# Optimization experiments

Measured on AMD Instinct MI355X. Metric: run time of the kernel, lower is better.

## Reference

```python
import jax, jax.numpy as jnp
import numpy as np

N = 20000      # nodes
E = 320000     # edges
C = 8          # n_species (input 0e multiplicity)
H = 128        # hidden multiplicity per irrep
RB = 8         # radial basis size
RM = 64        # radial mlp width
CUTOFF = 5.0
P = 2.0        # polynomial cutoff power
AVG_N = 16.0   # avg_n_neighbors
SQRT3 = float(np.sqrt(3.0))


def _w(k, i, o, scale=1.0):
    return jax.random.normal(k, (i, o), jnp.float32) * np.sqrt(scale / i)


def setup_inputs() -> dict:
    key = jax.random.key(0)
    ks = jax.random.split(key, 24)
    return {
        'displacements': jax.random.normal(ks[0], (E, 3), jnp.float32) * 1.5,
        'species': jax.random.randint(ks[1], (N,), 0, C, dtype=jnp.int32),
        'senders': jax.random.randint(ks[2], (E,), 0, N, dtype=jnp.int32),
        'receivers': jax.random.randint(ks[3], (E,), 0, N, dtype=jnp.int32),
        'l1_lin1': _w(ks[4], C, C),
        'l1_rw0': _w(ks[5], RB, RM, 4.0),
        'l1_rw1': _w(ks[6], RM, RM, 4.0),
        'l1_rw2': _w(ks[7], RM, RM, 4.0),
        'l1_rw3': _w(ks[8], RM, 2 * C),
        'l1_w2s': _w(ks[9], C, 2 * H),
        'l1_w2v': _w(ks[10], C, H),
        'l1_skip': jax.random.normal(ks[11], (C, C, 2 * H), jnp.float32) / np.sqrt(C),
        'l2_lin1s': _w(ks[12], H, H),
        'l2_lin1v': _w(ks[13], H, H),
        'l2_rw0': _w(ks[14], RB, RM, 4.0),
        'l2_rw1': _w(ks[15], RM, RM, 4.0),
        'l2_rw2': _w(ks[16], RM, RM, 4.0),
        'l2_rw3': _w(ks[17], RM, 2 * H),
        'l2_w2': _w(ks[18], 2 * H, H),
        'l2_skip': jax.random.normal(ks[19], (C, H, H), jnp.float32) / np.sqrt(H),
        'readout_w': _w(ks[20], H, 1),
    }


def _bessel(x):
    w = jnp.linspace(1.0, RB, RB) * jnp.pi
    xs = x[:, None]
    safe = jnp.where(xs == 0.0, 1.0, xs)
    return (2.0 / CUTOFF) * jnp.where(xs == 0.0, w / CUTOFF, jnp.sin(w * xs / CUTOFF) / safe)


def _poly_cutoff(x):
    u = x / CUTOFF
    out = 1.0 - (P + 1.0) * (P + 2.0) / 2.0 * u ** P \
        + P * (P + 2.0) * u ** (P + 1.0) \
        - P * (P + 1.0) / 2.0 * u ** (P + 2.0)
    return out * jnp.where(u < 1.0, 1.0, 0.0)


def _radial(rb, w0, w1, w2, w3):
    h = jax.nn.silu(rb @ w0)
    h = jax.nn.silu(h @ w1)
    h = jax.nn.silu(h @ w2)
    return h @ w3


def _node_energies(displacements, species, senders, receivers,
                   l1_lin1, l1_rw0, l1_rw1, l1_rw2, l1_rw3, l1_w2s, l1_w2v, l1_skip,
                   l2_lin1s, l2_lin1v, l2_rw0, l2_rw1, l2_rw2, l2_rw3, l2_w2, l2_skip,
                   readout_w):
    sq = jnp.sum(displacements ** 2, axis=-1)
    rn = jnp.where(sq == 0.0, 0.0, jnp.sqrt(jnp.where(sq == 0.0, 1.0, sq)))
    rb = _bessel(rn) * _poly_cutoff(rn)[:, None]                     # (E,RB)
    unit = displacements / jnp.where(rn == 0.0, 1.0, rn)[:, None]
    Y1 = SQRT3 * unit                                                # 1o SH, component norm
    onehot = jax.nn.one_hot(species, C, dtype=displacements.dtype)   # (N,C) = Cx0e features
    inv_sqrt_nbr = 1.0 / np.sqrt(AVG_N)

    # ---- layer 1: Cx0e -> 128x0e + 128x1o ----
    s = (onehot @ l1_lin1)[senders]                                  # (E,C)
    R = _radial(rb, l1_rw0, l1_rw1, l1_rw2, l1_rw3)                  # (E,2C)
    msg_s = s * R[:, :C]                                             # 0e x 0e -> 0e
    msg_v = s[:, :, None] * Y1[:, None, :] * R[:, C:, None]          # 0e x 1o -> 1o (E,C,3)
    agg_s = jax.ops.segment_sum(msg_s, receivers, num_segments=N) * inv_sqrt_nbr
    agg_v = jax.ops.segment_sum(msg_v, receivers, num_segments=N) * inv_sqrt_nbr
    scal = agg_s @ l1_w2s + jnp.einsum('nc,ncd->nd', onehot, l1_skip[species])  # (N,2H)
    vec = jnp.einsum('nci,cd->ndi', agg_v, l1_w2v)                   # (N,H,3)
    # gate: first H even scalars -> silu, last H scalars gate the 1o vectors
    x0 = jax.nn.silu(scal[:, :H])
    x1 = vec * jax.nn.silu(scal[:, H:])[:, :, None]

    # ---- layer 2: 128x0e + 128x1o -> 128x0e ----
    s2 = (x0 @ l2_lin1s)[senders]                                    # (E,H)
    v2 = jnp.einsum('nci,cd->ndi', x1, l2_lin1v)[senders]            # (E,H,3)
    tp = jnp.concatenate([s2, jnp.einsum('eci,ei->ec', v2, Y1) / SQRT3], axis=-1)  # (E,2H)
    R2 = _radial(rb, l2_rw0, l2_rw1, l2_rw2, l2_rw3)                 # (E,2H)
    agg2 = jax.ops.segment_sum(tp * R2, receivers, num_segments=N) * inv_sqrt_nbr
    feat = jax.nn.silu(agg2 @ l2_w2 + jnp.einsum('nc,ncd->nd', x0, l2_skip[species]))

    return feat @ readout_w                                          # (N,1) node energies


def reference(displacements, l1_lin1, l1_rw0, l1_rw1, l1_rw2, l1_rw3, l1_w2s, l1_w2v,
              l1_skip, l2_lin1s, l2_lin1v, l2_rw0, l2_rw1, l2_rw2, l2_rw3, l2_w2,
              l2_skip, readout_w, species, senders, receivers):
    return _node_energies(displacements, species, senders, receivers,
                          l1_lin1, l1_rw0, l1_rw1, l1_rw2, l1_rw3, l1_w2s, l1_w2v, l1_skip,
                          l2_lin1s, l2_lin1v, l2_rw0, l2_rw1, l2_rw2, l2_rw3, l2_w2, l2_skip,
                          readout_w)
```

## Files before the change

kernel.cpp:

```cpp
#include <hip/hip_runtime.h>
#include <math.h>

#define NN_ 20000
#define EE_ 320000
#define SHP 68

__device__ __forceinline__ float silu_f(float x) { return x / (1.0f + expf(-x)); }

template<int KD>
__device__ __forceinline__ void layer_step(float* __restrict__ sh_h,
                                           const float* __restrict__ sh_w,
                                           int wavebase, int eg, int jg) {
  const int jb = jg * 8;
  float acc[8][8];
#pragma unroll
  for (int ee = 0; ee < 8; ++ee)
#pragma unroll
    for (int jj = 0; jj < 8; ++jj) acc[ee][jj] = 0.f;

#pragma unroll
  for (int kc = 0; kc < KD; kc += 4) {
    float4 w4[4][2];
#pragma unroll
    for (int kk = 0; kk < 4; ++kk) {
      w4[kk][0] = *(const float4*)&sh_w[(kc + kk) * 64 + jb];
      w4[kk][1] = *(const float4*)&sh_w[(kc + kk) * 64 + jb + 4];
    }
    float4 h4[8];
#pragma unroll
    for (int ee = 0; ee < 8; ++ee)
      h4[ee] = *(const float4*)&sh_h[(wavebase + eg + 8 * ee) * SHP + kc];
#pragma unroll
    for (int kk = 0; kk < 4; ++kk) {
#pragma unroll
      for (int ee = 0; ee < 8; ++ee) {
        const float hv = ((const float*)&h4[ee])[kk];
        acc[ee][0] = fmaf(hv, w4[kk][0].x, acc[ee][0]);
        acc[ee][1] = fmaf(hv, w4[kk][0].y, acc[ee][1]);
        acc[ee][2] = fmaf(hv, w4[kk][0].z, acc[ee][2]);
        acc[ee][3] = fmaf(hv, w4[kk][0].w, acc[ee][3]);
        acc[ee][4] = fmaf(hv, w4[kk][1].x, acc[ee][4]);
        acc[ee][5] = fmaf(hv, w4[kk][1].y, acc[ee][5]);
        acc[ee][6] = fmaf(hv, w4[kk][1].z, acc[ee][6]);
        acc[ee][7] = fmaf(hv, w4[kk][1].w, acc[ee][7]);
      }
    }
  }
#pragma unroll
  for (int ee = 0; ee < 8; ++ee) {
    float* dst = &sh_h[(wavebase + eg + 8 * ee) * SHP + jb];
    float4 lo = {silu_f(acc[ee][0]), silu_f(acc[ee][1]), silu_f(acc[ee][2]), silu_f(acc[ee][3])};
    float4 hi = {silu_f(acc[ee][4]), silu_f(acc[ee][5]), silu_f(acc[ee][6]), silu_f(acc[ee][7])};
    *(float4*)dst = lo;
    *(float4*)(dst + 4) = hi;
  }
}

__device__ __forceinline__ void load_w(const float* __restrict__ W, int nfloat,
                                       float* __restrict__ dst, int t) {
  for (int i = t * 4; i < nfloat; i += 512) *(float4*)(dst + i) = *(const float4*)(W + i);
}

__global__ __launch_bounds__(256) void k_hist(const int* __restrict__ receivers,
                                              int* __restrict__ hist) {
  const int e = blockIdx.x * 256 + threadIdx.x;
  atomicAdd(&hist[receivers[e]], 1);
}

__global__ __launch_bounds__(1024) void k_scan(const int* __restrict__ hist,
                                               int* __restrict__ offs,
                                               int* __restrict__ cursor) {
  __shared__ int lds[1024];
  __shared__ int carry_s;
  const int t = threadIdx.x;
  if (t == 0) carry_s = 0;
  __syncthreads();
  for (int base = 0; base < NN_; base += 1024) {
    const int i = base + t;
    const int v = (i < NN_) ? hist[i] : 0;
    lds[t] = v;
    __syncthreads();
    for (int d = 1; d < 1024; d <<= 1) {
      const int tv = (t >= d) ? lds[t - d] : 0;
      __syncthreads();
      lds[t] += tv;
      __syncthreads();
    }
    const int inc = lds[t];
    const int c = carry_s;
    if (i < NN_) {
      const int off = c + inc - v;
      offs[i] = off;
      cursor[i] = off;
    }
    __syncthreads();
    if (t == 0) carry_s = c + lds[1023];
    __syncthreads();
  }
  if (t == 0) offs[NN_] = carry_s;
}

__global__ __launch_bounds__(256) void k_scatter(const int* __restrict__ receivers,
                                                 int* __restrict__ cursor,
                                                 int* __restrict__ edge_id) {
  const int e = blockIdx.x * 256 + threadIdx.x;
  const int r = receivers[e];
  const int pos = atomicAdd(&cursor[r], 1);
  edge_id[pos] = e;
}

__global__ __launch_bounds__(128) void k1a_radial(
    const float* __restrict__ disp, const int* __restrict__ species,
    const int* __restrict__ senders,
    const float* __restrict__ lin1,
    const float* __restrict__ rw0, const float* __restrict__ rw1,
    const float* __restrict__ rw2, const float* __restrict__ rw3,
    float* __restrict__ buf1, float* __restrict__ rbc_g, float* __restrict__ y1_g) {
  __shared__ float sh_h[128 * SHP];
  __shared__ float sh_w[64 * 64];
  const int t = threadIdx.x;
  const int e0 = blockIdx.x * 128;
  const int e = e0 + t;

  const float dx = disp[e * 3 + 0], dy = disp[e * 3 + 1], dz = disp[e * 3 + 2];
  const float sq = dx * dx + dy * dy + dz * dz;
  const float rn = sqrtf(sq);
  const float inv = (rn == 0.f) ? 1.f : (1.f / rn);
  const float u = rn * 0.2f;
  float fc;
  {
    const float u2 = u * u;
    fc = 1.f - 6.f * u2 + 8.f * u2 * u - 3.f * u2 * u2;
    fc = (u < 1.f) ? fc : 0.f;
  }
  float rb[8];
#pragma unroll
  for (int k = 0; k < 8; ++k) {
    const float wk = (float)(k + 1) * 3.14159265358979323846f;
    const float s = (rn == 0.f) ? (wk * 0.2f) : (sinf(wk * u) * inv);
    rb[k] = 0.4f * s * fc;
  }
  float4 r0 = {rb[0], rb[1], rb[2], rb[3]};
  float4 r1 = {rb[4], rb[5], rb[6], rb[7]};
  *(float4*)(rbc_g + e * 8) = r0;
  *(float4*)(rbc_g + e * 8 + 4) = r1;
  const float y1x = 1.7320508075688772f * dx * inv;
  const float y1y = 1.7320508075688772f * dy * inv;
  const float y1z = 1.7320508075688772f * dz * inv;
  float4 y4 = {y1x, y1y, y1z, 0.f};
  *(float4*)(y1_g + e * 4) = y4;
  *(float4*)&sh_h[t * SHP] = r0;
  *(float4*)&sh_h[t * SHP + 4] = r1;

  const int wavebase = (t >> 6) * 64;
  const int lane = t & 63;
  const int eg = lane >> 3, jg = lane & 7;

  load_w(rw0, 8 * 64, sh_w, t);
  __syncthreads();
  layer_step<8>(sh_h, sh_w, wavebase, eg, jg);
  __syncthreads();
  load_w(rw1, 64 * 64, sh_w, t);
  __syncthreads();
  layer_step<64>(sh_h, sh_w, wavebase, eg, jg);
  __syncthreads();
  load_w(rw2, 64 * 64, sh_w, t);
  __syncthreads();
  layer_step<64>(sh_h, sh_w, wavebase, eg, jg);
  __syncthreads();

  float R[16];
#pragma unroll
  for (int c = 0; c < 16; ++c) R[c] = 0.f;
  for (int k = 0; k < 64; ++k) {
    const float h = sh_h[t * SHP + k];
#pragma unroll
    for (int c = 0; c < 16; ++c) R[c] = fmaf(h, rw3[k * 16 + c], R[c]);
  }

  const int sp = species[senders[e]];
  float m[32];
#pragma unroll
  for (int c = 0; c < 8; ++c) {
    const float sc = lin1[sp * 8 + c];
    m[c] = sc * R[c];
    const float mv = sc * R[8 + c];
    m[8 + c * 3 + 0] = mv * y1x;
    m[8 + c * 3 + 1] = mv * y1y;
    m[8 + c * 3 + 2] = mv * y1z;
  }
  float* dst = buf1 + (size_t)e * 32;
#pragma unroll
  for (int q = 0; q < 8; ++q) {
    float4 v = {m[q * 4 + 0], m[q * 4 + 1], m[q * 4 + 2], m[q * 4 + 3]};
    *(float4*)(dst + q * 4) = v;
  }
}

__global__ __launch_bounds__(128) void k3a_radial(
    const float* __restrict__ rbc_g,
    const float* __restrict__ rw0, const float* __restrict__ rw1,
    const float* __restrict__ rw2,
    float* __restrict__ ha_buf) {
  __shared__ float sh_h[128 * SHP];
  __shared__ float sh_w[64 * 64];
  const int t = threadIdx.x;
  const int e0 = blockIdx.x * 128;

  *(float4*)&sh_h[t * SHP] = *(const float4*)(rbc_g + (size_t)(e0 + t) * 8);
  *(float4*)&sh_h[t * SHP + 4] = *(const float4*)(rbc_g + (size_t)(e0 + t) * 8 + 4);

  const int wavebase = (t >> 6) * 64;
  const int lane = t & 63;
  const int eg = lane >> 3, jg = lane & 7;

  load_w(rw0, 8 * 64, sh_w, t);
  __syncthreads();
  layer_step<8>(sh_h, sh_w, wavebase, eg, jg);
  __syncthreads();
  load_w(rw1, 64 * 64, sh_w, t);
  __syncthreads();
  layer_step<64>(sh_h, sh_w, wavebase, eg, jg);
  __syncthreads();
  load_w(rw2, 64 * 64, sh_w, t);
  __syncthreads();
  layer_step<64>(sh_h, sh_w, wavebase, eg, jg);
  __syncthreads();

#pragma unroll
  for (int r = 0; r < 16; ++r) {
    const int lin = r * 128 + t;
    const int el = lin >> 4;
    const int k = (lin & 15) * 4;
    *(float4*)(ha_buf + (size_t)(e0 + el) * 64 + k) = *(const float4*)&sh_h[el * SHP + k];
  }
}

__global__ __launch_bounds__(256) void k1b_gather(
    const float* __restrict__ buf1, const int* __restrict__ offs,
    const int* __restrict__ edge_id,
    float* __restrict__ agg_s, float* __restrict__ agg_v) {
  const int n = blockIdx.x * 8 + (threadIdx.x >> 5);
  const int ch = threadIdx.x & 31;
  const int beg = offs[n], end = offs[n + 1];
  float acc = 0.f;
  for (int i = beg; i < end; ++i) {
    const int eid = edge_id[i];
    acc += buf1[(size_t)eid * 32 + ch];
  }
  if (ch < 8) agg_s[n * 8 + ch] = acc;
  else agg_v[n * 24 + (ch - 8)] = acc;
}

__global__ __launch_bounds__(64) void k2a_node(
    const float* __restrict__ agg_s, const float* __restrict__ agg_v,
    const int* __restrict__ species,
    const float* __restrict__ w2s, const float* __restrict__ w2v,
    const float* __restrict__ skip1,
    float* __restrict__ x0_g, float* __restrict__ x1_g) {
  const int n = blockIdx.x;
  const int l = threadIdx.x;
  __shared__ float g_lds[128];
  const int sp = species[n];
  float as[8];
#pragma unroll
  for (int k = 0; k < 8; ++k) as[k] = agg_s[n * 8 + k] * 0.25f;
  float sc[4];
#pragma unroll
  for (int j = 0; j < 4; ++j) {
    const int d = l * 4 + j;
    float a = skip1[(sp * 9) * 256 + d];
#pragma unroll
    for (int k = 0; k < 8; ++k) a = fmaf(as[k], w2s[k * 256 + d], a);
    sc[j] = silu_f(a);
  }
  if (l < 32) {
#pragma unroll
    for (int j = 0; j < 4; ++j) x0_g[n * 128 + l * 4 + j] = sc[j];
  } else {
#pragma unroll
    for (int j = 0; j < 4; ++j) g_lds[(l - 32) * 4 + j] = sc[j];
  }
  __syncthreads();
  float av[24];
#pragma unroll
  for (int k = 0; k < 24; ++k) av[k] = agg_v[n * 24 + k] * 0.25f;
#pragma unroll
  for (int h = 0; h < 2; ++h) {
    const int d = l + h * 64;
    const float g = g_lds[d];
    float v0 = 0.f, v1 = 0.f, v2v = 0.f;
#pragma unroll
    for (int c = 0; c < 8; ++c) {
      const float w = w2v[c * 128 + d];
      v0 = fmaf(av[c * 3 + 0], w, v0);
      v1 = fmaf(av[c * 3 + 1], w, v1);
      v2v = fmaf(av[c * 3 + 2], w, v2v);
    }
    x1_g[(n * 3 + 0) * 128 + d] = v0 * g;
    x1_g[(n * 3 + 1) * 128 + d] = v1 * g;
    x1_g[(n * 3 + 2) * 128 + d] = v2v * g;
  }
}

__global__ __launch_bounds__(256) void k2b_gemm(
    const float* __restrict__ x0_g, const float* __restrict__ x1_g,
    const int* __restrict__ species,
    const float* __restrict__ lin1s, const float* __restrict__ lin1v,
    const float* __restrict__ skip2,
    float* __restrict__ s2_g, float* __restrict__ v2_g,
    float* __restrict__ skipv_g) {
  const int w = __builtin_amdgcn_readfirstlane((int)(threadIdx.x >> 6));
  const int l = threadIdx.x & 63;
  const int nbase = blockIdx.x * 32 + w * 8;
  float s2a[8] = {}, s2b[8] = {}, ska[8] = {}, skb[8] = {};
  float v2a[8][3] = {}, v2b[8][3] = {};
  int sp[8];
#pragma unroll
  for (int nn = 0; nn < 8; ++nn) sp[nn] = species[nbase + nn];
  for (int c = 0; c < 128; ++c) {
    const float wA0 = lin1s[c * 128 + l];
    const float wA1 = lin1s[c * 128 + 64 + l];
    const float wB0 = lin1v[c * 128 + l];
    const float wB1 = lin1v[c * 128 + 64 + l];
#pragma unroll
    for (int nn = 0; nn < 8; ++nn) {
      const int n = nbase + nn;
      const float x0v = x0_g[n * 128 + c];
      const float wS0 = skip2[sp[nn] * 16384 + c * 128 + l];
      const float wS1 = skip2[sp[nn] * 16384 + c * 128 + 64 + l];
      s2a[nn] = fmaf(x0v, wA0, s2a[nn]);
      s2b[nn] = fmaf(x0v, wA1, s2b[nn]);
      ska[nn] = fmaf(x0v, wS0, ska[nn]);
      skb[nn] = fmaf(x0v, wS1, skb[nn]);
#pragma unroll
      for (int i = 0; i < 3; ++i) {
        const float x1v = x1_g[(n * 3 + i) * 128 + c];
        v2a[nn][i] = fmaf(x1v, wB0, v2a[nn][i]);
        v2b[nn][i] = fmaf(x1v, wB1, v2b[nn][i]);
      }
    }
  }
#pragma unroll
  for (int nn = 0; nn < 8; ++nn) {
    const int n = nbase + nn;
    s2_g[n * 128 + l] = s2a[nn];
    s2_g[n * 128 + 64 + l] = s2b[nn];
    skipv_g[n * 128 + l] = ska[nn];
    skipv_g[n * 128 + 64 + l] = skb[nn];
#pragma unroll
    for (int i = 0; i < 3; ++i) {
      v2_g[n * 384 + l * 3 + i] = v2a[nn][i];
      v2_g[n * 384 + (64 + l) * 3 + i] = v2b[nn][i];
    }
  }
}

__global__ __launch_bounds__(256) void k3b_gather(
    const float* __restrict__ ha_buf, const float* __restrict__ y1_g,
    const int* __restrict__ senders,
    const int* __restrict__ offs, const int* __restrict__ edge_id,
    const float* __restrict__ rw3,
    const float* __restrict__ s2_g, const float* __restrict__ v2_g,
    float* __restrict__ agg2) {
  const int n = blockIdx.x;
  const int ch = threadIdx.x;
  float w[64];
#pragma unroll
  for (int k = 0; k < 64; ++k) w[k] = rw3[k * 256 + ch];
  const int beg = offs[n], end = offs[n + 1];
  const bool is_s = ch < 128;
  const int c3 = (ch - 128) * 3;
  float acc = 0.f;
  for (int i = beg; i < end; ++i) {
    const int eid = __builtin_amdgcn_readfirstlane(edge_id[i]);
    const int s = __builtin_amdgcn_readfirstlane(senders[eid]);
    const float y1x = y1_g[eid * 4 + 0];
    const float y1y = y1_g[eid * 4 + 1];
    const float y1z = y1_g[eid * 4 + 2];
    float tp;
    if (is_s) {
      tp = s2_g[(size_t)s * 128 + ch];
    } else {
      tp = (v2_g[(size_t)s * 384 + c3 + 0] * y1x +
            v2_g[(size_t)s * 384 + c3 + 1] * y1y +
            v2_g[(size_t)s * 384 + c3 + 2] * y1z) * 0.5773502691896258f;
    }
    const float* ha = ha_buf + (size_t)eid * 64;
    float r0 = 0.f, r1 = 0.f, r2 = 0.f, r3 = 0.f;
#pragma unroll
    for (int k = 0; k < 64; k += 4) {
      r0 = fmaf(ha[k + 0], w[k + 0], r0);
      r1 = fmaf(ha[k + 1], w[k + 1], r1);
      r2 = fmaf(ha[k + 2], w[k + 2], r2);
      r3 = fmaf(ha[k + 3], w[k + 3], r3);
    }
    acc = fmaf(tp, (r0 + r1) + (r2 + r3), acc);
  }
  agg2[(size_t)n * 256 + ch] = acc;
}

__global__ __launch_bounds__(256) void k4_node(
    const float* __restrict__ agg2, const float* __restrict__ skipv,
    const float* __restrict__ w2, const float* __restrict__ readout,
    float* __restrict__ out) {
  __shared__ float tile[64 * 65];
  __shared__ float partial[256];
  const int t = threadIdx.x;
  const int w = __builtin_amdgcn_readfirstlane((int)(threadIdx.x >> 6));
  const int l = t & 63;
  const int n0 = blockIdx.x * 64;
  const int n = n0 + l;
  float acc[32];
#pragma unroll
  for (int j = 0; j < 32; ++j) acc[j] = 0.f;
  for (int ko = 0; ko < 256; ko += 64) {
    __syncthreads();
#pragma unroll
    for (int rep = 0; rep < 16; ++rep) {
      const int lin = rep * 256 + t;
      const int node = lin >> 6, kk = lin & 63;
      const int gn = n0 + node;
      tile[kk * 65 + node] = (gn < NN_) ? agg2[(size_t)gn * 256 + ko + kk] * 0.25f : 0.f;
    }
    __syncthreads();
    for (int kk = 0; kk < 64; ++kk) {
      const float a = tile[kk * 65 + l];
#pragma unroll
      for (int jj = 0; jj < 32; ++jj)
        acc[jj] = fmaf(a, w2[(ko + kk) * 128 + w * 32 + jj], acc[jj]);
    }
  }
  float po = 0.f;
  if (n < NN_) {
#pragma unroll
    for (int jj = 0; jj < 32; ++jj) {
      const int d = w * 32 + jj;
      const float v = acc[jj] + skipv[n * 128 + d];
      po = fmaf(silu_f(v), readout[d], po);
    }
  }
  partial[w * 64 + l] = po;
  __syncthreads();
  if (t < 64 && n0 + t < NN_) {
    out[n0 + t] = partial[t] + partial[64 + t] + partial[128 + t] + partial[192 + t];
  }
}

extern "C" void kernel_launch(void* const* d_in, const int* in_sizes, int n_in,
                              void* d_out, int out_size, void* d_ws, size_t ws_size,
                              hipStream_t stream) {
  const float* disp = (const float*)d_in[0];
  const int* species = (const int*)d_in[1];
  const int* senders = (const int*)d_in[2];
  const int* receivers = (const int*)d_in[3];
  const float* l1_lin1 = (const float*)d_in[4];
  const float* l1_rw0 = (const float*)d_in[5];
  const float* l1_rw1 = (const float*)d_in[6];
  const float* l1_rw2 = (const float*)d_in[7];
  const float* l1_rw3 = (const float*)d_in[8];
  const float* l1_w2s = (const float*)d_in[9];
  const float* l1_w2v = (const float*)d_in[10];
  const float* l1_skip = (const float*)d_in[11];
  const float* l2_lin1s = (const float*)d_in[12];
  const float* l2_lin1v = (const float*)d_in[13];
  const float* l2_rw0 = (const float*)d_in[14];
  const float* l2_rw1 = (const float*)d_in[15];
  const float* l2_rw2 = (const float*)d_in[16];
  const float* l2_rw3 = (const float*)d_in[17];
  const float* l2_w2 = (const float*)d_in[18];
  const float* l2_skip = (const float*)d_in[19];
  const float* readout_w = (const float*)d_in[20];

  float* ws = (float*)d_ws;
  float* rbc   = ws;
  float* y1    = ws + 2560000;
  float* s2    = ws + 3840000;
  float* v2    = ws + 6400000;
  float* skipv = ws + 14080000;
  float* agg2  = ws + 16640000;
  float* pool  = ws + 21760000;
  float* agg_s = pool;
  float* agg_v = pool + 160000;
  float* buf1  = pool + 640000;
  float* x0    = pool + 640000;
  float* x1    = pool + 3200000;
  float* ha    = pool;
  int* ibase   = (int*)(ws + 42240000);
  int* hist    = ibase;
  int* cursor  = ibase + 20000;
  int* offs    = ibase + 40000;
  int* edge_id = ibase + 60001;
  if (ws_size < (size_t)(42240000 + 380001) * 4) return;

  hipMemsetAsync(hist, 0, 20000 * sizeof(int), stream);
  k_hist<<<EE_ / 256, 256, 0, stream>>>(receivers, hist);
  k_scan<<<1, 1024, 0, stream>>>(hist, offs, cursor);
  k_scatter<<<EE_ / 256, 256, 0, stream>>>(receivers, cursor, edge_id);

  k1a_radial<<<EE_ / 128, 128, 0, stream>>>(disp, species, senders, l1_lin1,
                                            l1_rw0, l1_rw1, l1_rw2, l1_rw3,
                                            buf1, rbc, y1);
  k1b_gather<<<NN_ / 8, 256, 0, stream>>>(buf1, offs, edge_id, agg_s, agg_v);
  k2a_node<<<NN_, 64, 0, stream>>>(agg_s, agg_v, species, l1_w2s, l1_w2v, l1_skip,
                                   x0, x1);
  k2b_gemm<<<NN_ / 32, 256, 0, stream>>>(x0, x1, species, l2_lin1s, l2_lin1v,
                                         l2_skip, s2, v2, skipv);

  k3a_radial<<<EE_ / 128, 128, 0, stream>>>(rbc, l2_rw0, l2_rw1, l2_rw2, ha);
  k3b_gather<<<NN_, 256, 0, stream>>>(ha, y1, senders, offs, edge_id, l2_rw3,
                                      s2, v2, agg2);
  k4_node<<<(NN_ + 63) / 64, 256, 0, stream>>>(agg2, skipv, l2_w2, readout_w,
                                               (float*)d_out);
}
```

Baseline: 1.092 ms.

## Stage per-edge radial hidden rows in LDS in batches of sixteen edges

The layer-2 gather kernel now loads the 64-wide hidden radial activations for up to 16 incoming edges cooperatively into shared memory with float4 loads. Each thread then reads them back as broadcast float4 LDS reads instead of every thread issuing scalar global loads per edge. The sender feature gathers for all 16 edges are issued before the compute loop so more memory requests are in flight at once. The cost is two block barriers per batch, extra registers for the tp array and the pinned float4 weights, and wasted lanes when a node has few neighbours.

```diff
diff --git a/kernel.cpp b/kernel.cpp
--- a/kernel.cpp
+++ b/kernel.cpp
@@ -6,6 +6,8 @@
 #define SHP 68
 
 __device__ __forceinline__ float silu_f(float x) { return x / (1.0f + expf(-x)); }
+
+#define KEEP4(v) asm volatile("" : "+v"(v.x), "+v"(v.y), "+v"(v.z), "+v"(v.w))
 
 template<int KD>
 __device__ __forceinline__ void layer_step(float* __restrict__ sh_h,
@@ -363,39 +365,71 @@
     const float* __restrict__ rw3,
     const float* __restrict__ s2_g, const float* __restrict__ v2_g,
     float* __restrict__ agg2) {
+  __shared__ float ha_lds[16][64];
   const int n = blockIdx.x;
   const int ch = threadIdx.x;
-  float w[64];
-#pragma unroll
-  for (int k = 0; k < 64; ++k) w[k] = rw3[k * 256 + ch];
+
+  float4 w4[16];
+#pragma unroll
+  for (int q = 0; q < 16; ++q) {
+    w4[q].x = rw3[(q * 4 + 0) * 256 + ch];
+    w4[q].y = rw3[(q * 4 + 1) * 256 + ch];
+    w4[q].z = rw3[(q * 4 + 2) * 256 + ch];
+    w4[q].w = rw3[(q * 4 + 3) * 256 + ch];
+    KEEP4(w4[q]);
+  }
+
   const int beg = offs[n], end = offs[n + 1];
   const bool is_s = ch < 128;
   const int c3 = (ch - 128) * 3;
+  const int be = ch >> 4;
+  const int k4 = (ch & 15) * 4;
   float acc = 0.f;
-  for (int i = beg; i < end; ++i) {
-    const int eid = __builtin_amdgcn_readfirstlane(edge_id[i]);
-    const int s = __builtin_amdgcn_readfirstlane(senders[eid]);
-    const float y1x = y1_g[eid * 4 + 0];
-    const float y1y = y1_g[eid * 4 + 1];
-    const float y1z = y1_g[eid * 4 + 2];
-    float tp;
-    if (is_s) {
-      tp = s2_g[(size_t)s * 128 + ch];
-    } else {
-      tp = (v2_g[(size_t)s * 384 + c3 + 0] * y1x +
-            v2_g[(size_t)s * 384 + c3 + 1] * y1y +
-            v2_g[(size_t)s * 384 + c3 + 2] * y1z) * 0.5773502691896258f;
-    }
-    const float* ha = ha_buf + (size_t)eid * 64;
-    float r0 = 0.f, r1 = 0.f, r2 = 0.f, r3 = 0.f;
-#pragma unroll
-    for (int k = 0; k < 64; k += 4) {
-      r0 = fmaf(ha[k + 0], w[k + 0], r0);
-      r1 = fmaf(ha[k + 1], w[k + 1], r1);
-      r2 = fmaf(ha[k + 2], w[k + 2], r2);
-      r3 = fmaf(ha[k + 3], w[k + 3], r3);
-    }
-    acc = fmaf(tp, (r0 + r1) + (r2 + r3), acc);
+
+  for (int b = beg; b < end; b += 16) {
+    const int nb = end - b;
+    __syncthreads();
+    float4 hv = {0.f, 0.f, 0.f, 0.f};
+    if (be < nb) {
+      const int eid = edge_id[b + be];
+      hv = *(const float4*)(ha_buf + (size_t)eid * 64 + k4);
+    }
+    *(float4*)&ha_lds[be][k4] = hv;
+    float tp[16];
+#pragma unroll
+    for (int j = 0; j < 16; ++j) {
+      tp[j] = 0.f;
+      if (j < nb) {
+        const int eid = __builtin_amdgcn_readfirstlane(edge_id[b + j]);
+        const int s = __builtin_amdgcn_readfirstlane(senders[eid]);
+        if (is_s) {
+          tp[j] = s2_g[(size_t)s * 128 + ch];
+        } else {
+          const float y1x = y1_g[eid * 4 + 0];
+          const float y1y = y1_g[eid * 4 + 1];
+          const float y1z = y1_g[eid * 4 + 2];
+          tp[j] = (v2_g[(size_t)s * 384 + c3 + 0] * y1x +
+                   v2_g[(size_t)s * 384 + c3 + 1] * y1y +
+                   v2_g[(size_t)s * 384 + c3 + 2] * y1z) * 0.5773502691896258f;
+        }
+      }
+    }
+    __syncthreads();
+#pragma unroll
+    for (int j = 0; j < 16; ++j) {
+      if (j < nb) {
+        float d0 = 0.f, d1 = 0.f, d2 = 0.f, d3 = 0.f;
+#pragma unroll
+        for (int q = 0; q < 16; ++q) {
+          const float4 h = *(const float4*)&ha_lds[j][q * 4];
+          d0 = fmaf(h.x, w4[q].x, d0);
+          d1 = fmaf(h.y, w4[q].y, d1);
+          d2 = fmaf(h.z, w4[q].z, d2);
+          d3 = fmaf(h.w, w4[q].w, d3);
+        }
+        acc = fmaf(tp[j], (d0 + d1) + (d2 + d3), acc);
+      }
+    }
   }
   agg2[(size_t)n * 256 + ch] = acc;
 }
```

Result: slower. 1.410 ms (+29.1%).

## Move final radial layer into tiled GEMM and process edges in sorted phases

Applied to the files above, without the earlier changes.

The last radial-MLP layer (64->256) no longer runs as a per-edge register dot product inside the gather kernel. It now runs as a shared-memory tiled GEMM in the radial kernel, which reads edges in receiver-sorted order and writes the full 256-wide R2 rows to a buffer. Because that buffer is large, edges are handled in four phases of 80000. Each phase launches the radial GEMM and then a gather that adds each node's partial sums into a zeroed agg2. The aim is to remove the redundant per-node, per-channel 64-FMA work and the 64-register weight array in the gather, at the cost of about 80MB of extra R2 traffic per phase, eight extra launches, a memset and read-modify-write accumulation into agg2.

```diff
diff --git a/kernel.cpp b/kernel.cpp
--- a/kernel.cpp
+++ b/kernel.cpp
@@ -4,6 +4,7 @@
 #define NN_ 20000
 #define EE_ 320000
 #define SHP 68
+#define EPH 80000
 
 __device__ __forceinline__ float silu_f(float x) { return x / (1.0f + expf(-x)); }
 
@@ -51,6 +52,55 @@
     float* dst = &sh_h[(wavebase + eg + 8 * ee) * SHP + jb];
     float4 lo = {silu_f(acc[ee][0]), silu_f(acc[ee][1]), silu_f(acc[ee][2]), silu_f(acc[ee][3])};
     float4 hi = {silu_f(acc[ee][4]), silu_f(acc[ee][5]), silu_f(acc[ee][6]), silu_f(acc[ee][7])};
+    *(float4*)dst = lo;
+    *(float4*)(dst + 4) = hi;
+  }
+}
+
+__device__ __forceinline__ void gemm_chunk_out(const float* __restrict__ sh_h,
+                                               const float* __restrict__ sh_w,
+                                               int wavebase, int eg, int jg,
+                                               float* __restrict__ dst_base) {
+  const int jb = jg * 8;
+  float acc[8][8];
+#pragma unroll
+  for (int ee = 0; ee < 8; ++ee)
+#pragma unroll
+    for (int jj = 0; jj < 8; ++jj) acc[ee][jj] = 0.f;
+
+#pragma unroll
+  for (int kc = 0; kc < 64; kc += 4) {
+    float4 w4[4][2];
+#pragma unroll
+    for (int kk = 0; kk < 4; ++kk) {
+      w4[kk][0] = *(const float4*)&sh_w[(kc + kk) * 64 + jb];
+      w4[kk][1] = *(const float4*)&sh_w[(kc + kk) * 64 + jb + 4];
+    }
+    float4 h4[8];
+#pragma unroll
+    for (int ee = 0; ee < 8; ++ee)
+      h4[ee] = *(const float4*)&sh_h[(wavebase + eg + 8 * ee) * SHP + kc];
+#pragma unroll
+    for (int kk = 0; kk < 4; ++kk) {
+#pragma unroll
+      for (int ee = 0; ee < 8; ++ee) {
+        const float hv = ((const float*)&h4[ee])[kk];
+        acc[ee][0] = fmaf(hv, w4[kk][0].x, acc[ee][0]);
+        acc[ee][1] = fmaf(hv, w4[kk][0].y, acc[ee][1]);
+        acc[ee][2] = fmaf(hv, w4[kk][0].z, acc[ee][2]);
+        acc[ee][3] = fmaf(hv, w4[kk][0].w, acc[ee][3]);
+        acc[ee][4] = fmaf(hv, w4[kk][1].x, acc[ee][4]);
+        acc[ee][5] = fmaf(hv, w4[kk][1].y, acc[ee][5]);
+        acc[ee][6] = fmaf(hv, w4[kk][1].z, acc[ee][6]);
+        acc[ee][7] = fmaf(hv, w4[kk][1].w, acc[ee][7]);
+      }
+    }
+  }
+#pragma unroll
+  for (int ee = 0; ee < 8; ++ee) {
+    float* dst = dst_base + (size_t)(wavebase + eg + 8 * ee) * 256 + jb;
+    float4 lo = {acc[ee][0], acc[ee][1], acc[ee][2], acc[ee][3]};
+    float4 hi = {acc[ee][4], acc[ee][5], acc[ee][6], acc[ee][7]};
     *(float4*)dst = lo;
     *(float4*)(dst + 4) = hi;
   }
@@ -197,18 +247,19 @@
   }
 }
 
-__global__ __launch_bounds__(128) void k3a_radial(
-    const float* __restrict__ rbc_g,
+__global__ __launch_bounds__(128) void k3a_fused(
+    const float* __restrict__ rbc_g, const int* __restrict__ edge_id,
     const float* __restrict__ rw0, const float* __restrict__ rw1,
-    const float* __restrict__ rw2,
-    float* __restrict__ ha_buf) {
+    const float* __restrict__ rw2, const float* __restrict__ rw3,
+    float* __restrict__ r2buf, int pbase) {
   __shared__ float sh_h[128 * SHP];
   __shared__ float sh_w[64 * 64];
   const int t = threadIdx.x;
-  const int e0 = blockIdx.x * 128;
-
-  *(float4*)&sh_h[t * SHP] = *(const float4*)(rbc_g + (size_t)(e0 + t) * 8);
-  *(float4*)&sh_h[t * SHP + 4] = *(const float4*)(rbc_g + (size_t)(e0 + t) * 8 + 4);
+  const int p = pbase + blockIdx.x * 128 + t;
+  const int eid = edge_id[p];
+
+  *(float4*)&sh_h[t * SHP] = *(const float4*)(rbc_g + (size_t)eid * 8);
+  *(float4*)&sh_h[t * SHP + 4] = *(const float4*)(rbc_g + (size_t)eid * 8 + 4);
 
   const int wavebase = (t >> 6) * 64;
   const int lane = t & 63;
@@ -225,15 +276,52 @@
   load_w(rw2, 64 * 64, sh_w, t);
   __syncthreads();
   layer_step<64>(sh_h, sh_w, wavebase, eg, jg);
-  __syncthreads();
-
-#pragma unroll
-  for (int r = 0; r < 16; ++r) {
-    const int lin = r * 128 + t;
-    const int el = lin >> 4;
-    const int k = (lin & 15) * 4;
-    *(float4*)(ha_buf + (size_t)(e0 + el) * 64 + k) = *(const float4*)&sh_h[el * SHP + k];
-  }
+
+  float* block_base = r2buf + (size_t)(blockIdx.x * 128) * 256;
+  for (int c = 0; c < 4; ++c) {
+    __syncthreads();
+    for (int i = t * 4; i < 4096; i += 512) {
+      const int row = i >> 6, col = i & 63;
+      *(float4*)&sh_w[i] = *(const float4*)&rw3[row * 256 + c * 64 + col];
+    }
+    __syncthreads();
+    gemm_chunk_out(sh_h, sh_w, wavebase, eg, jg, block_base + c * 64);
+  }
+}
+
+__global__ __launch_bounds__(256) void k3b_phase(
+    const float* __restrict__ r2buf, const float* __restrict__ y1_g,
+    const int* __restrict__ senders,
+    const int* __restrict__ offs, const int* __restrict__ edge_id,
+    const float* __restrict__ s2_g, const float* __restrict__ v2_g,
+    float* __restrict__ agg2, int pbase, int pend) {
+  const int n = blockIdx.x;
+  const int ch = threadIdx.x;
+  const int beg = offs[n], end = offs[n + 1];
+  const int lo = beg > pbase ? beg : pbase;
+  const int hi = end < pend ? end : pend;
+  if (lo >= hi) return;
+  const bool is_s = ch < 128;
+  const int c3 = (ch - 128) * 3;
+  float acc = 0.f;
+  for (int i = lo; i < hi; ++i) {
+    const int eid = __builtin_amdgcn_readfirstlane(edge_id[i]);
+    const int s = __builtin_amdgcn_readfirstlane(senders[eid]);
+    const float rv = r2buf[(size_t)(i - pbase) * 256 + ch];
+    float tp;
+    if (is_s) {
+      tp = s2_g[(size_t)s * 128 + ch];
+    } else {
+      const float y1x = y1_g[eid * 4 + 0];
+      const float y1y = y1_g[eid * 4 + 1];
+      const float y1z = y1_g[eid * 4 + 2];
+      tp = (v2_g[(size_t)s * 384 + c3 + 0] * y1x +
+            v2_g[(size_t)s * 384 + c3 + 1] * y1y +
+            v2_g[(size_t)s * 384 + c3 + 2] * y1z) * 0.5773502691896258f;
+    }
+    acc = fmaf(tp, rv, acc);
+  }
+  agg2[(size_t)n * 256 + ch] += acc;
 }
 
 __global__ __launch_bounds__(256) void k1b_gather(
@@ -354,50 +442,6 @@
       v2_g[n * 384 + (64 + l) * 3 + i] = v2b[nn][i];
     }
   }
-}
-
-__global__ __launch_bounds__(256) void k3b_gather(
-    const float* __restrict__ ha_buf, const float* __restrict__ y1_g,
-    const int* __restrict__ senders,
-    const int* __restrict__ offs, const int* __restrict__ edge_id,
-    const float* __restrict__ rw3,
-    const float* __restrict__ s2_g, const float* __restrict__ v2_g,
-    float* __restrict__ agg2) {
-  const int n = blockIdx.x;
-  const int ch = threadIdx.x;
-  float w[64];
-#pragma unroll
-  for (int k = 0; k < 64; ++k) w[k] = rw3[k * 256 + ch];
-  const int beg = offs[n], end = offs[n + 1];
-  const bool is_s = ch < 128;
-  const int c3 = (ch - 128) * 3;
-  float acc = 0.f;
-  for (int i = beg; i < end; ++i) {
-    const int eid = __builtin_amdgcn_readfirstlane(edge_id[i]);
-    const int s = __builtin_amdgcn_readfirstlane(senders[eid]);
-    const float y1x = y1_g[eid * 4 + 0];
-    const float y1y = y1_g[eid * 4 + 1];
-    const float y1z = y1_g[eid * 4 + 2];
-    float tp;
-    if (is_s) {
-      tp = s2_g[(size_t)s * 128 + ch];
-    } else {
-      tp = (v2_g[(size_t)s * 384 + c3 + 0] * y1x +
-            v2_g[(size_t)s * 384 + c3 + 1] * y1y +
-            v2_g[(size_t)s * 384 + c3 + 2] * y1z) * 0.5773502691896258f;
-    }
-    const float* ha = ha_buf + (size_t)eid * 64;
-    float r0 = 0.f, r1 = 0.f, r2 = 0.f, r3 = 0.f;
-#pragma unroll
-    for (int k = 0; k < 64; k += 4) {
-      r0 = fmaf(ha[k + 0], w[k + 0], r0);
-      r1 = fmaf(ha[k + 1], w[k + 1], r1);
-      r2 = fmaf(ha[k + 2], w[k + 2], r2);
-      r3 = fmaf(ha[k + 3], w[k + 3], r3);
-    }
-    acc = fmaf(tp, (r0 + r1) + (r2 + r3), acc);
-  }
-  agg2[(size_t)n * 256 + ch] = acc;
 }
 
 __global__ __launch_bounds__(256) void k4_node(
@@ -485,7 +529,7 @@
   float* buf1  = pool + 640000;
   float* x0    = pool + 640000;
   float* x1    = pool + 3200000;
-  float* ha    = pool;
+  float* r2    = pool;
   int* ibase   = (int*)(ws + 42240000);
   int* hist    = ibase;
   int* cursor  = ibase + 20000;
@@ -494,6 +538,8 @@
   if (ws_size < (size_t)(42240000 + 380001) * 4) return;
 
   hipMemsetAsync(hist, 0, 20000 * sizeof(int), stream);
+  hipMemsetAsync(agg2, 0, (size_t)5120000 * sizeof(float), stream);
+
   k_hist<<<EE_ / 256, 256, 0, stream>>>(receivers, hist);
   k_scan<<<1, 1024, 0, stream>>>(hist, offs, cursor);
   k_scatter<<<EE_ / 256, 256, 0, stream>>>(receivers, cursor, edge_id);
@@ -507,9 +553,12 @@
   k2b_gemm<<<NN_ / 32, 256, 0, stream>>>(x0, x1, species, l2_lin1s, l2_lin1v,
                                          l2_skip, s2, v2, skipv);
 
-  k3a_radial<<<EE_ / 128, 128, 0, stream>>>(rbc, l2_rw0, l2_rw1, l2_rw2, ha);
-  k3b_gather<<<NN_, 256, 0, stream>>>(ha, y1, senders, offs, edge_id, l2_rw3,
-                                      s2, v2, agg2);
+  for (int q = 0; q < 4; ++q) {
+    k3a_fused<<<EPH / 128, 128, 0, stream>>>(rbc, edge_id, l2_rw0, l2_rw1, l2_rw2,
+                                             l2_rw3, r2, EPH * q);
+    k3b_phase<<<NN_, 256, 0, stream>>>(r2, y1, senders, offs, edge_id, s2, v2,
+                                       agg2, EPH * q, EPH * (q + 1));
+  }
   k4_node<<<(NN_ + 63) / 64, 256, 0, stream>>>(agg2, skipv, l2_w2, readout_w,
                                                (float*)d_out);
 }
```

New measurement: 2.517 ms. +130.6%, slower.
